# Kernel optimization log

Hardware: AMD Instinct MI355X
Metric: run time of the kernel (lower is better)

Reference implementation:

```python
import jax, jax.numpy as jnp
import numpy as np

N_INPUT = 1024
BATCH = 65536


def setup_inputs() -> dict:
    key = jax.random.key(0)
    kx, kA, kB = jax.random.split(key, 3)
    # average half must be strictly positive for pow(average, alpha)
    x = jax.random.uniform(kx, (BATCH, 2 * N_INPUT), dtype=jnp.float32,
                           minval=0.1, maxval=2.0)
    A = jax.random.normal(kA, (N_INPUT,), dtype=jnp.float32)
    B = jax.random.normal(kB, (N_INPUT, N_INPUT), dtype=jnp.float32)
    C = jnp.zeros((1,), dtype=jnp.float32)
    alpha = jnp.ones((N_INPUT,), dtype=jnp.float32)
    return {"x": x, "A": A, "B": B, "C": C, "alpha": alpha}


def reference(x, A, B, C, alpha):
    n = A.shape[0]
    average = x[:, :n]          # [batch, n]
    numbers = x[:, -n:]         # [batch, n]
    organelle = numbers * jnp.power(average, alpha)  # [batch, n]
    linear = organelle @ A                                   # [batch]
    quad = jnp.einsum('bi,ij,bj->b', organelle, B, organelle)  # batched quadratic form
    return linear + quad + C    # C broadcasts [1] -> [batch]
```

## Files before the change

kernel.cpp:

```cpp
#include <hip/hip_runtime.h>
#include <hip/hip_bf16.h>

typedef __bf16 bf16x8 __attribute__((ext_vector_type(8)));
typedef __bf16 bf16x4 __attribute__((ext_vector_type(4)));
typedef float  f32x4  __attribute__((ext_vector_type(4)));

#define N_IN 1024
#define BM   64
#define NTHR 512

__global__ void convB_kernel(const float* __restrict__ B, __bf16* __restrict__ Bb) {
    int i = blockIdx.x * blockDim.x + threadIdx.x;
    f32x4 v = ((const f32x4*)B)[i];
    bf16x4 o;
    o[0] = (__bf16)v[0]; o[1] = (__bf16)v[1]; o[2] = (__bf16)v[2]; o[3] = (__bf16)v[3];
    ((bf16x4*)Bb)[i] = o;
}

template<bool USEBF>
__global__ __launch_bounds__(NTHR, 2)
void fused_kernel(const float* __restrict__ x, const float* __restrict__ A,
                  const float* __restrict__ Bf, const __bf16* __restrict__ Bb,
                  const float* __restrict__ Cp, const float* __restrict__ alpha,
                  float* __restrict__ out) {
    __shared__ __align__(16) __bf16 o_panel[BM * N_IN];
    __shared__ float rowsum[8][BM];

    const int t    = threadIdx.x;
    const int wave = t >> 6;
    const int lane = t & 63;
    const int lrow = lane & 15;
    const int lgrp = lane >> 4;
    const long blk_row = (long)blockIdx.x * BM;

    const int srow  = t >> 3;
    const int skoff = (t & 7) * 4;
    const float* xrow = x + (blk_row + srow) * (2 * N_IN);

    #pragma unroll
    for (int c = 0; c < 8; ++c) {
        int k = c * 32 + skoff;
        f32x4 sa  = *(const f32x4*)(xrow + k);
        f32x4 sn  = *(const f32x4*)(xrow + N_IN + k);
        f32x4 sal = *(const f32x4*)(alpha + k);
        bf16x4 w4;
        #pragma unroll
        for (int e = 0; e < 4; ++e)
            w4[e] = (__bf16)(sn[e] * __expf(sal[e] * __logf(sa[e])));
        *(bf16x4*)&o_panel[srow * N_IN + ((k & ~7) ^ ((srow & 7) << 3)) + (k & 7)] = w4;
    }
    __syncthreads();

    f32x4 acc[2][4][4];
    #pragma unroll
    for (int h = 0; h < 2; ++h)
        #pragma unroll
        for (int m = 0; m < 4; ++m)
            #pragma unroll
            for (int n = 0; n < 4; ++n)
                acc[h][m][n] = f32x4{0.f, 0.f, 0.f, 0.f};

    #pragma unroll 1
    for (int q = 0; q < 4; ++q) {
        #pragma unroll
        for (int kq = 0; kq < 8; ++kq) {
            const int kc = q * 8 + kq;
            const bool staging = (q < 3);
            const int kk = kc * 32 + lgrp * 8;

            bf16x8 bfr[2][4];
            #pragma unroll
            for (int h = 0; h < 2; ++h)
                #pragma unroll
                for (int n = 0; n < 4; ++n) {
                    int i = h * 512 + wave * 64 + n * 16 + lrow;
                    if constexpr (USEBF) {
                        bfr[h][n] = *(const bf16x8*)&Bb[(long)i * N_IN + kk];
                    } else {
                        const float* p = Bf + (long)i * N_IN + kk;
                        f32x4 lo = *(const f32x4*)p;
                        f32x4 hi = *(const f32x4*)(p + 4);
                        #pragma unroll
                        for (int e = 0; e < 4; ++e) {
                            bfr[h][n][e]     = (__bf16)lo[e];
                            bfr[h][n][e + 4] = (__bf16)hi[e];
                        }
                    }
                }

            f32x4 sa, sn, sal;
            if (staging) {
                int k = (kc + 8) * 32 + skoff;
                sa  = *(const f32x4*)(xrow + k);
                sn  = *(const f32x4*)(xrow + N_IN + k);
                sal = *(const f32x4*)(alpha + k);
            }

            bf16x8 afr[4];
            #pragma unroll
            for (int m = 0; m < 4; ++m) {
                int r = m * 16 + lrow;
                afr[m] = *(const bf16x8*)&o_panel[r * N_IN + (kk ^ ((r & 7) << 3))];
            }

            #pragma unroll
            for (int h = 0; h < 2; ++h)
                #pragma unroll
                for (int m = 0; m < 4; ++m)
                    #pragma unroll
                    for (int n = 0; n < 4; ++n)
                        acc[h][m][n] = __builtin_amdgcn_mfma_f32_16x16x32_bf16(
                            afr[m], bfr[h][n], acc[h][m][n], 0, 0, 0);

            if (staging) {
                int k = (kc + 8) * 32 + skoff;
                bf16x4 w4;
                #pragma unroll
                for (int e = 0; e < 4; ++e)
                    w4[e] = (__bf16)(sn[e] * __expf(sal[e] * __logf(sa[e])));
                *(bf16x4*)&o_panel[srow * N_IN + ((k & ~7) ^ ((srow & 7) << 3)) + (k & 7)] = w4;
            }
        }
        __syncthreads();
    }

    float rowpart[16];
    #pragma unroll
    for (int i = 0; i < 16; ++i) rowpart[i] = 0.f;
    #pragma unroll
    for (int h = 0; h < 2; ++h)
        #pragma unroll
        for (int n = 0; n < 4; ++n) {
            int i = h * 512 + wave * 64 + n * 16 + lrow;
            float Ai = A[i];
            #pragma unroll
            for (int m = 0; m < 4; ++m)
                #pragma unroll
                for (int j = 0; j < 4; ++j) {
                    int r = m * 16 + lgrp * 4 + j;
                    float y  = acc[h][m][n][j] + Ai;
                    float ov = (float)o_panel[r * N_IN + ((i & ~7) ^ ((r & 7) << 3)) + (i & 7)];
                    rowpart[m * 4 + j] += y * ov;
                }
        }

    #pragma unroll
    for (int d = 1; d < 16; d <<= 1) {
        #pragma unroll
        for (int i = 0; i < 16; ++i)
            rowpart[i] += __shfl_xor(rowpart[i], d);
    }
    if (lrow == 0) {
        #pragma unroll
        for (int m = 0; m < 4; ++m)
            #pragma unroll
            for (int j = 0; j < 4; ++j)
                rowsum[wave][m * 16 + lgrp * 4 + j] = rowpart[m * 4 + j];
    }
    __syncthreads();
    if (t < BM) {
        float s = Cp[0];
        #pragma unroll
        for (int w = 0; w < 8; ++w) s += rowsum[w][t];
        out[blk_row + t] = s;
    }
}

extern "C" void kernel_launch(void* const* d_in, const int* in_sizes, int n_in,
                              void* d_out, int out_size, void* d_ws, size_t ws_size,
                              hipStream_t stream) {
    const float* x     = (const float*)d_in[0];
    const float* A     = (const float*)d_in[1];
    const float* B     = (const float*)d_in[2];
    const float* C     = (const float*)d_in[3];
    const float* alpha = (const float*)d_in[4];
    float* out = (float*)d_out;

    int batch = in_sizes[0] / (2 * N_IN);
    int grid  = batch / BM;

    bool useBf = (ws_size >= (size_t)(N_IN * N_IN * sizeof(__bf16)));
    if (useBf) {
        __bf16* Bb = (__bf16*)d_ws;
        int nvec = (N_IN * N_IN) / 4;
        convB_kernel<<<nvec / 256, 256, 0, stream>>>(B, Bb);
        fused_kernel<true><<<grid, NTHR, 0, stream>>>(x, A, nullptr, Bb, C, alpha, out);
    } else {
        fused_kernel<false><<<grid, NTHR, 0, stream>>>(x, A, B, nullptr, C, alpha, out);
    }
}
```

Baseline: 446.6 us.

## Halve row tile to 32 and target four blocks per CU

The batch tile drops from 64 to 32 rows, so the LDS panel halves to 64 KB and the launch bound asks for 4 blocks per SM instead of 2. Each wave now owns 128 contiguous output columns (8 N-tiles × 2 M-tiles) instead of 2×4×4, which cuts accumulator registers. Staging loads shrink to float2 per thread. The goal is higher occupancy and better latency hiding, at the cost of reading the B matrix twice as often per batch row, which lowers arithmetic intensity for the bf16 B stream.

```diff
diff --git a/kernel.cpp b/kernel.cpp
--- a/kernel.cpp
+++ b/kernel.cpp
@@ -2,23 +2,26 @@
 #include <hip/hip_bf16.h>
 
 typedef __bf16 bf16x8 __attribute__((ext_vector_type(8)));
-typedef __bf16 bf16x4 __attribute__((ext_vector_type(4)));
+typedef __bf16 bf16x2 __attribute__((ext_vector_type(2)));
 typedef float  f32x4  __attribute__((ext_vector_type(4)));
+typedef float  f32x2  __attribute__((ext_vector_type(2)));
 
 #define N_IN 1024
-#define BM   64
+#define BM   32
 #define NTHR 512
 
 __global__ void convB_kernel(const float* __restrict__ B, __bf16* __restrict__ Bb) {
     int i = blockIdx.x * blockDim.x + threadIdx.x;
     f32x4 v = ((const f32x4*)B)[i];
-    bf16x4 o;
-    o[0] = (__bf16)v[0]; o[1] = (__bf16)v[1]; o[2] = (__bf16)v[2]; o[3] = (__bf16)v[3];
-    ((bf16x4*)Bb)[i] = o;
+    __bf16 o0 = (__bf16)v[0], o1 = (__bf16)v[1], o2 = (__bf16)v[2], o3 = (__bf16)v[3];
+    bf16x2 p0; p0[0] = o0; p0[1] = o1;
+    bf16x2 p1; p1[0] = o2; p1[1] = o3;
+    ((bf16x2*)Bb)[2 * i]     = p0;
+    ((bf16x2*)Bb)[2 * i + 1] = p1;
 }
 
 template<bool USEBF>
-__global__ __launch_bounds__(NTHR, 2)
+__global__ __launch_bounds__(NTHR, 4)
 void fused_kernel(const float* __restrict__ x, const float* __restrict__ A,
                   const float* __restrict__ Bf, const __bf16* __restrict__ Bb,
                   const float* __restrict__ Cp, const float* __restrict__ alpha,
@@ -33,32 +36,31 @@
     const int lgrp = lane >> 4;
     const long blk_row = (long)blockIdx.x * BM;
 
-    const int srow  = t >> 3;
-    const int skoff = (t & 7) * 4;
+    const int srow  = t >> 4;
+    const int skoff = (t & 15) * 2;
     const float* xrow = x + (blk_row + srow) * (2 * N_IN);
+    const int ssw   = (srow & 7) << 3;
+    const int sbase = srow * N_IN;
 
     #pragma unroll
     for (int c = 0; c < 8; ++c) {
         int k = c * 32 + skoff;
-        f32x4 sa  = *(const f32x4*)(xrow + k);
-        f32x4 sn  = *(const f32x4*)(xrow + N_IN + k);
-        f32x4 sal = *(const f32x4*)(alpha + k);
-        bf16x4 w4;
-        #pragma unroll
-        for (int e = 0; e < 4; ++e)
-            w4[e] = (__bf16)(sn[e] * __expf(sal[e] * __logf(sa[e])));
-        *(bf16x4*)&o_panel[srow * N_IN + ((k & ~7) ^ ((srow & 7) << 3)) + (k & 7)] = w4;
+        f32x2 sa  = *(const f32x2*)(xrow + k);
+        f32x2 sn  = *(const f32x2*)(xrow + N_IN + k);
+        f32x2 sal = *(const f32x2*)(alpha + k);
+        bf16x2 w2;
+        w2[0] = (__bf16)(sn[0] * __expf(sal[0] * __logf(sa[0])));
+        w2[1] = (__bf16)(sn[1] * __expf(sal[1] * __logf(sa[1])));
+        *(bf16x2*)&o_panel[sbase + ((k & ~7) ^ ssw) + (k & 7)] = w2;
     }
     __syncthreads();
 
-    f32x4 acc[2][4][4];
+    f32x4 acc[2][8];
     #pragma unroll
-    for (int h = 0; h < 2; ++h)
+    for (int m = 0; m < 2; ++m)
         #pragma unroll
-        for (int m = 0; m < 4; ++m)
-            #pragma unroll
-            for (int n = 0; n < 4; ++n)
-                acc[h][m][n] = f32x4{0.f, 0.f, 0.f, 0.f};
+        for (int n = 0; n < 8; ++n)
+            acc[m][n] = f32x4{0.f, 0.f, 0.f, 0.f};
 
     #pragma unroll 1
     for (int q = 0; q < 4; ++q) {
@@ -68,94 +70,87 @@
             const bool staging = (q < 3);
             const int kk = kc * 32 + lgrp * 8;
 
-            bf16x8 bfr[2][4];
-            #pragma unroll
-            for (int h = 0; h < 2; ++h)
-                #pragma unroll
-                for (int n = 0; n < 4; ++n) {
-                    int i = h * 512 + wave * 64 + n * 16 + lrow;
-                    if constexpr (USEBF) {
-                        bfr[h][n] = *(const bf16x8*)&Bb[(long)i * N_IN + kk];
-                    } else {
-                        const float* p = Bf + (long)i * N_IN + kk;
-                        f32x4 lo = *(const f32x4*)p;
-                        f32x4 hi = *(const f32x4*)(p + 4);
-                        #pragma unroll
-                        for (int e = 0; e < 4; ++e) {
-                            bfr[h][n][e]     = (__bf16)lo[e];
-                            bfr[h][n][e + 4] = (__bf16)hi[e];
-                        }
-                    }
-                }
-
-            f32x4 sa, sn, sal;
+            f32x2 sa, sn, sal;
             if (staging) {
                 int k = (kc + 8) * 32 + skoff;
-                sa  = *(const f32x4*)(xrow + k);
-                sn  = *(const f32x4*)(xrow + N_IN + k);
-                sal = *(const f32x4*)(alpha + k);
+                sa  = *(const f32x2*)(xrow + k);
+                sn  = *(const f32x2*)(xrow + N_IN + k);
+                sal = *(const f32x2*)(alpha + k);
             }
 
-            bf16x8 afr[4];
+            bf16x8 afr[2];
             #pragma unroll
-            for (int m = 0; m < 4; ++m) {
+            for (int m = 0; m < 2; ++m) {
                 int r = m * 16 + lrow;
                 afr[m] = *(const bf16x8*)&o_panel[r * N_IN + (kk ^ ((r & 7) << 3))];
             }
 
+            bf16x8 bfr[8];
             #pragma unroll
-            for (int h = 0; h < 2; ++h)
+            for (int n = 0; n < 8; ++n) {
+                int i = wave * 128 + n * 16 + lrow;
+                if constexpr (USEBF) {
+                    bfr[n] = *(const bf16x8*)&Bb[(long)i * N_IN + kk];
+                } else {
+                    const float* p = Bf + (long)i * N_IN + kk;
+                    f32x4 lo = *(const f32x4*)p;
+                    f32x4 hi = *(const f32x4*)(p + 4);
+                    #pragma unroll
+                    for (int e = 0; e < 4; ++e) {
+                        bfr[n][e]     = (__bf16)lo[e];
+                        bfr[n][e + 4] = (__bf16)hi[e];
+                    }
+                }
+            }
+
+            #pragma unroll
+            for (int m = 0; m < 2; ++m)
                 #pragma unroll
-                for (int m = 0; m < 4; ++m)
-                    #pragma unroll
-                    for (int n = 0; n < 4; ++n)
-                        acc[h][m][n] = __builtin_amdgcn_mfma_f32_16x16x32_bf16(
-                            afr[m], bfr[h][n], acc[h][m][n], 0, 0, 0);
+                for (int n = 0; n < 8; ++n)
+                    acc[m][n] = __builtin_amdgcn_mfma_f32_16x16x32_bf16(
+                        afr[m], bfr[n], acc[m][n], 0, 0, 0);
 
             if (staging) {
                 int k = (kc + 8) * 32 + skoff;
-                bf16x4 w4;
-                #pragma unroll
-                for (int e = 0; e < 4; ++e)
-                    w4[e] = (__bf16)(sn[e] * __expf(sal[e] * __logf(sa[e])));
-                *(bf16x4*)&o_panel[srow * N_IN + ((k & ~7) ^ ((srow & 7) << 3)) + (k & 7)] = w4;
+                bf16x2 w2;
+                w2[0] = (__bf16)(sn[0] * __expf(sal[0] * __logf(sa[0])));
+                w2[1] = (__bf16)(sn[1] * __expf(sal[1] * __logf(sa[1])));
+                *(bf16x2*)&o_panel[sbase + ((k & ~7) ^ ssw) + (k & 7)] = w2;
             }
         }
         __syncthreads();
     }
 
-    float rowpart[16];
+    float rp[8];
     #pragma unroll
-    for (int i = 0; i < 16; ++i) rowpart[i] = 0.f;
+    for (int i = 0; i < 8; ++i) rp[i] = 0.f;
     #pragma unroll
-    for (int h = 0; h < 2; ++h)
+    for (int n = 0; n < 8; ++n) {
+        int i = wave * 128 + n * 16 + lrow;
+        float Ai = A[i];
         #pragma unroll
-        for (int n = 0; n < 4; ++n) {
-            int i = h * 512 + wave * 64 + n * 16 + lrow;
-            float Ai = A[i];
+        for (int m = 0; m < 2; ++m)
             #pragma unroll
-            for (int m = 0; m < 4; ++m)
-                #pragma unroll
-                for (int j = 0; j < 4; ++j) {
-                    int r = m * 16 + lgrp * 4 + j;
-                    float y  = acc[h][m][n][j] + Ai;
-                    float ov = (float)o_panel[r * N_IN + ((i & ~7) ^ ((r & 7) << 3)) + (i & 7)];
-                    rowpart[m * 4 + j] += y * ov;
-                }
-        }
+            for (int j = 0; j < 4; ++j) {
+                int r = m * 16 + lgrp * 4 + j;
+                float y  = acc[m][n][j] + Ai;
+                float ov = (float)o_panel[r * N_IN + ((i & ~7) ^ ((r & 7) << 3)) + (i & 7)];
+                rp[m * 4 + j] += y * ov;
+            }
+    }
 
     #pragma unroll
     for (int d = 1; d < 16; d <<= 1) {
         #pragma unroll
-        for (int i = 0; i < 16; ++i)
-            rowpart[i] += __shfl_xor(rowpart[i], d);
+        for (int i = 0; i < 8; ++i)
+            rp[i] += __shfl_xor(rp[i], d);
     }
     if (lrow == 0) {
         #pragma unroll
-        for (int m = 0; m < 4; ++m)
+        for (int m = 0; m < 2; ++m)
             #pragma unroll
             for (int j = 0; j < 4; ++j)
-                rowsum[wave][m * 16 + lgrp * 4 + j] = rowpart[m * 4 + j];
+                rowsum[wave][m * 16 + lgrp * 4 + j] = rp[m * 4 + j];
     }
     __syncthreads();
     if (t < BM) {
```

After: 939.8 us. 110% more time.

## Split pow into separate kernel and double-buffer B loads in new quadratic-form kernel

Applied to the files above, without the earlier changes.

Adds a standalone pow_kernel that writes the bf16 organelle matrix to workspace, and a qf_kernel that loads it into LDS and runs the MFMA loop with 128 output columns per wave and register double-buffered B fragments. This moves the transcendental staging out of the MFMA loop and drops the per-quarter barriers. In exchange it adds an extra global write and read of a batch x 1024 bf16 buffer (128 MB) and needs a larger workspace, falling back to the fused kernel otherwise.

```diff
diff --git a/kernel.cpp b/kernel.cpp
--- a/kernel.cpp
+++ b/kernel.cpp
@@ -3,7 +3,9 @@
 
 typedef __bf16 bf16x8 __attribute__((ext_vector_type(8)));
 typedef __bf16 bf16x4 __attribute__((ext_vector_type(4)));
+typedef __bf16 bf16x2 __attribute__((ext_vector_type(2)));
 typedef float  f32x4  __attribute__((ext_vector_type(4)));
+typedef float  f32x2  __attribute__((ext_vector_type(2)));
 
 #define N_IN 1024
 #define BM   64
@@ -15,6 +17,132 @@
     bf16x4 o;
     o[0] = (__bf16)v[0]; o[1] = (__bf16)v[1]; o[2] = (__bf16)v[2]; o[3] = (__bf16)v[3];
     ((bf16x4*)Bb)[i] = o;
+}
+
+__global__ __launch_bounds__(256)
+void pow_kernel(const float* __restrict__ x, const float* __restrict__ alpha,
+                __bf16* __restrict__ O, int nvec) {
+    for (int v = blockIdx.x * blockDim.x + threadIdx.x; v < nvec;
+         v += gridDim.x * blockDim.x) {
+        int row = v >> 7;
+        int k   = (v & 127) << 3;
+        const float* xr = x + (long)row * (2 * N_IN);
+        f32x4 a0 = *(const f32x4*)(xr + k);
+        f32x4 a1 = *(const f32x4*)(xr + k + 4);
+        f32x4 n0 = *(const f32x4*)(xr + N_IN + k);
+        f32x4 n1 = *(const f32x4*)(xr + N_IN + k + 4);
+        f32x4 l0 = *(const f32x4*)(alpha + k);
+        f32x4 l1 = *(const f32x4*)(alpha + k + 4);
+        bf16x8 w;
+        #pragma unroll
+        for (int e = 0; e < 4; ++e) {
+            w[e]     = (__bf16)(n0[e] * __expf(l0[e] * __logf(a0[e])));
+            w[e + 4] = (__bf16)(n1[e] * __expf(l1[e] * __logf(a1[e])));
+        }
+        *(bf16x8*)(O + (long)row * N_IN + k) = w;
+    }
+}
+
+__global__ __launch_bounds__(NTHR, 2)
+void qf_kernel(const __bf16* __restrict__ O, const __bf16* __restrict__ Bb,
+               const float* __restrict__ A, const float* __restrict__ Cp,
+               float* __restrict__ out) {
+    __shared__ __align__(16) __bf16 o_panel[BM * N_IN];
+    __shared__ float rowsum[8][BM];
+
+    const int t    = threadIdx.x;
+    const int wave = t >> 6;
+    const int lane = t & 63;
+    const int lrow = lane & 15;
+    const int lgrp = lane >> 4;
+    const long blk_row = (long)blockIdx.x * BM;
+    const __bf16* Orow = O + blk_row * N_IN;
+
+    {
+        const int srow  = t >> 3;
+        const int sk    = (t & 7) * 8;
+        const int sw    = (srow & 7) << 3;
+        #pragma unroll
+        for (int c = 0; c < 16; ++c) {
+            int k = c * 64 + sk;
+            bf16x8 v = *(const bf16x8*)(Orow + (long)srow * N_IN + k);
+            *(bf16x8*)&o_panel[srow * N_IN + (k ^ sw)] = v;
+        }
+    }
+    __syncthreads();
+
+    f32x4 acc[4][8];
+    #pragma unroll
+    for (int m = 0; m < 4; ++m)
+        #pragma unroll
+        for (int n = 0; n < 8; ++n)
+            acc[m][n] = f32x4{0.f, 0.f, 0.f, 0.f};
+
+    const __bf16* bbase = Bb + (long)(wave * 128 + lrow) * N_IN + lgrp * 8;
+    auto loadB = [&](bf16x8* dst, int kc) {
+        #pragma unroll
+        for (int n = 0; n < 8; ++n)
+            dst[n] = *(const bf16x8*)(bbase + (long)n * 16 * N_IN + kc * 32);
+    };
+
+    bf16x8 b0[8], b1[8];
+    loadB(b0, 0);
+    loadB(b1, 1);
+
+    #pragma unroll 2
+    for (int kc = 0; kc < 32; ++kc) {
+        bf16x8* cur = (kc & 1) ? b1 : b0;
+        const int kk = kc * 32 + lgrp * 8;
+        bf16x8 afr[4];
+        #pragma unroll
+        for (int m = 0; m < 4; ++m) {
+            int r = m * 16 + lrow;
+            afr[m] = *(const bf16x8*)&o_panel[r * N_IN + (kk ^ ((r & 7) << 3))];
+        }
+        #pragma unroll
+        for (int m = 0; m < 4; ++m)
+            #pragma unroll
+            for (int n = 0; n < 8; ++n)
+                acc[m][n] = __builtin_amdgcn_mfma_f32_16x16x32_bf16(
+                    afr[m], cur[n], acc[m][n], 0, 0, 0);
+        if (kc + 2 < 32) loadB(cur, kc + 2);
+    }
+
+    float rp[16];
+    #pragma unroll
+    for (int i = 0; i < 16; ++i) rp[i] = 0.f;
+    #pragma unroll
+    for (int n = 0; n < 8; ++n) {
+        const int i = wave * 128 + n * 16 + lrow;
+        const float Ai = A[i];
+        #pragma unroll
+        for (int m = 0; m < 4; ++m)
+            #pragma unroll
+            for (int j = 0; j < 4; ++j) {
+                const int r = m * 16 + lgrp * 4 + j;
+                float ov = (float)o_panel[r * N_IN + ((i & ~7) ^ ((r & 7) << 3)) + (i & 7)];
+                rp[m * 4 + j] += (acc[m][n][j] + Ai) * ov;
+            }
+    }
+    #pragma unroll
+    for (int d = 1; d < 16; d <<= 1)
+        #pragma unroll
+        for (int i = 0; i < 16; ++i)
+            rp[i] += __shfl_xor(rp[i], d);
+    if (lrow == 0) {
+        #pragma unroll
+        for (int m = 0; m < 4; ++m)
+            #pragma unroll
+            for (int j = 0; j < 4; ++j)
+                rowsum[wave][m * 16 + lgrp * 4 + j] = rp[m * 4 + j];
+    }
+    __syncthreads();
+    if (t < BM) {
+        float s = Cp[0];
+        #pragma unroll
+        for (int w = 0; w < 8; ++w) s += rowsum[w][t];
+        out[blk_row + t] = s;
+    }
 }
 
 template<bool USEBF>
@@ -25,23 +153,16 @@
                   float* __restrict__ out) {
     __shared__ __align__(16) __bf16 o_panel[BM * N_IN];
     __shared__ float rowsum[8][BM];
-
-    const int t    = threadIdx.x;
-    const int wave = t >> 6;
-    const int lane = t & 63;
-    const int lrow = lane & 15;
-    const int lgrp = lane >> 4;
+    const int t = threadIdx.x, wave = t >> 6, lane = t & 63;
+    const int lrow = lane & 15, lgrp = lane >> 4;
     const long blk_row = (long)blockIdx.x * BM;
-
-    const int srow  = t >> 3;
-    const int skoff = (t & 7) * 4;
+    const int srow = t >> 3, skoff = (t & 7) * 4;
     const float* xrow = x + (blk_row + srow) * (2 * N_IN);
-
     #pragma unroll
     for (int c = 0; c < 8; ++c) {
         int k = c * 32 + skoff;
-        f32x4 sa  = *(const f32x4*)(xrow + k);
-        f32x4 sn  = *(const f32x4*)(xrow + N_IN + k);
+        f32x4 sa = *(const f32x4*)(xrow + k);
+        f32x4 sn = *(const f32x4*)(xrow + N_IN + k);
         f32x4 sal = *(const f32x4*)(alpha + k);
         bf16x4 w4;
         #pragma unroll
@@ -50,7 +171,6 @@
         *(bf16x4*)&o_panel[srow * N_IN + ((k & ~7) ^ ((srow & 7) << 3)) + (k & 7)] = w4;
     }
     __syncthreads();
-
     f32x4 acc[2][4][4];
     #pragma unroll
     for (int h = 0; h < 2; ++h)
@@ -59,7 +179,6 @@
             #pragma unroll
             for (int n = 0; n < 4; ++n)
                 acc[h][m][n] = f32x4{0.f, 0.f, 0.f, 0.f};
-
     #pragma unroll 1
     for (int q = 0; q < 4; ++q) {
         #pragma unroll
@@ -67,7 +186,19 @@
             const int kc = q * 8 + kq;
             const bool staging = (q < 3);
             const int kk = kc * 32 + lgrp * 8;
-
+            f32x4 sa, sn, sal;
+            if (staging) {
+                int k = (kc + 8) * 32 + skoff;
+                sa = *(const f32x4*)(xrow + k);
+                sn = *(const f32x4*)(xrow + N_IN + k);
+                sal = *(const f32x4*)(alpha + k);
+            }
+            bf16x8 afr[4];
+            #pragma unroll
+            for (int m = 0; m < 4; ++m) {
+                int r = m * 16 + lrow;
+                afr[m] = *(const bf16x8*)&o_panel[r * N_IN + (kk ^ ((r & 7) << 3))];
+            }
             bf16x8 bfr[2][4];
             #pragma unroll
             for (int h = 0; h < 2; ++h)
@@ -82,27 +213,11 @@
                         f32x4 hi = *(const f32x4*)(p + 4);
                         #pragma unroll
                         for (int e = 0; e < 4; ++e) {
-                            bfr[h][n][e]     = (__bf16)lo[e];
+                            bfr[h][n][e] = (__bf16)lo[e];
                             bfr[h][n][e + 4] = (__bf16)hi[e];
                         }
                     }
                 }
-
-            f32x4 sa, sn, sal;
-            if (staging) {
-                int k = (kc + 8) * 32 + skoff;
-                sa  = *(const f32x4*)(xrow + k);
-                sn  = *(const f32x4*)(xrow + N_IN + k);
-                sal = *(const f32x4*)(alpha + k);
-            }
-
-            bf16x8 afr[4];
-            #pragma unroll
-            for (int m = 0; m < 4; ++m) {
-                int r = m * 16 + lrow;
-                afr[m] = *(const bf16x8*)&o_panel[r * N_IN + (kk ^ ((r & 7) << 3))];
-            }
-
             #pragma unroll
             for (int h = 0; h < 2; ++h)
                 #pragma unroll
@@ -111,7 +226,6 @@
                     for (int n = 0; n < 4; ++n)
                         acc[h][m][n] = __builtin_amdgcn_mfma_f32_16x16x32_bf16(
                             afr[m], bfr[h][n], acc[h][m][n], 0, 0, 0);
-
             if (staging) {
                 int k = (kc + 8) * 32 + skoff;
                 bf16x4 w4;
@@ -123,7 +237,6 @@
         }
         __syncthreads();
     }
-
     float rowpart[16];
     #pragma unroll
     for (int i = 0; i < 16; ++i) rowpart[i] = 0.f;
@@ -138,18 +251,16 @@
                 #pragma unroll
                 for (int j = 0; j < 4; ++j) {
                     int r = m * 16 + lgrp * 4 + j;
-                    float y  = acc[h][m][n][j] + Ai;
+                    float y = acc[h][m][n][j] + Ai;
                     float ov = (float)o_panel[r * N_IN + ((i & ~7) ^ ((r & 7) << 3)) + (i & 7)];
                     rowpart[m * 4 + j] += y * ov;
                 }
         }
-
-    #pragma unroll
-    for (int d = 1; d < 16; d <<= 1) {
+    #pragma unroll
+    for (int d = 1; d < 16; d <<= 1)
         #pragma unroll
         for (int i = 0; i < 16; ++i)
             rowpart[i] += __shfl_xor(rowpart[i], d);
-    }
     if (lrow == 0) {
         #pragma unroll
         for (int m = 0; m < 4; ++m)
@@ -176,16 +287,22 @@
     const float* alpha = (const float*)d_in[4];
     float* out = (float*)d_out;
 
-    int batch = in_sizes[0] / (2 * N_IN);
-    int grid  = batch / BM;
-
-    bool useBf = (ws_size >= (size_t)(N_IN * N_IN * sizeof(__bf16)));
-    if (useBf) {
+    const int batch = in_sizes[0] / (2 * N_IN);
+    const size_t bb_bytes = (size_t)N_IN * N_IN * 2;
+    const size_t o_bytes  = (size_t)batch * N_IN * 2;
+
+    if (ws_size >= bb_bytes + o_bytes) {
         __bf16* Bb = (__bf16*)d_ws;
-        int nvec = (N_IN * N_IN) / 4;
-        convB_kernel<<<nvec / 256, 256, 0, stream>>>(B, Bb);
-        fused_kernel<true><<<grid, NTHR, 0, stream>>>(x, A, nullptr, Bb, C, alpha, out);
+        __bf16* O  = (__bf16*)((char*)d_ws + bb_bytes);
+        convB_kernel<<<(N_IN * N_IN / 4) / 256, 256, 0, stream>>>(B, Bb);
+        int nvec = batch * (N_IN / 8);
+        pow_kernel<<<2048, 256, 0, stream>>>(x, alpha, O, nvec);
+        qf_kernel<<<batch / BM, NTHR, 0, stream>>>(O, Bb, A, C, out);
+    } else if (ws_size >= bb_bytes) {
+        __bf16* Bb = (__bf16*)d_ws;
+        convB_kernel<<<(N_IN * N_IN / 4) / 256, 256, 0, stream>>>(B, Bb);
+        fused_kernel<true><<<batch / BM, NTHR, 0, stream>>>(x, A, nullptr, Bb, C, alpha, out);
     } else {
-        fused_kernel<false><<<grid, NTHR, 0, stream>>>(x, A, B, nullptr, C, alpha, out);
-    }
-}
+        fused_kernel<false><<<batch / BM, NTHR, 0, stream>>>(x, A, B, nullptr, C, alpha, out);
+    }
+}
```

Result: faster. 391.1 us (-12.4%).
